# Optimization experiments

Hardware: AMD Instinct MI355X
Metric: run time of the kernel (lower is better)

## Reference

```python
import jax, jax.numpy as jnp
import numpy as np

EXTENT = 1.0  # kernel-point influence radius (init kwarg 'extent')
B, N, M, H, K, F, C = 4, 16384, 16384, 32, 15, 64, 64


def setup_inputs() -> dict:
    key = jax.random.key(0)
    ks = jax.random.split(key, 6)
    points = jax.random.uniform(ks[0], (B, N, 3), dtype=jnp.float32)
    features = jax.random.normal(ks[1], (B, N, F), dtype=jnp.float32)
    output_points = jax.random.uniform(ks[2], (B, M, 3), dtype=jnp.float32)
    neighbor_indices = jax.random.randint(ks[3], (B, M, H), 0, N)
    # kernel point dispositions inside a ball of radius 1.5*extent (load_kernels stand-in)
    k_points = jax.random.uniform(ks[4], (K, 3), minval=-1.0, maxval=1.0, dtype=jnp.float32) * (1.5 * EXTENT) / jnp.sqrt(3.0)
    k_values = jax.random.normal(ks[5], (K, F, C), dtype=jnp.float32) * 0.05
    return {
        'points': points, 'features': features, 'output_points': output_points,
        'k_points': k_points, 'k_values': k_values, 'neighbor_indices': neighbor_indices,
    }


def reference(points, features, output_points, k_points, k_values, neighbor_indices):
    b, m, h = neighbor_indices.shape
    idx = neighbor_indices.reshape(b, m * h, 1)
    # batched gather (tf.gather batch_dims=1)
    neigh_pts = jnp.take_along_axis(points, idx, axis=1).reshape(b, m, h, 3)
    neigh_feat = jnp.take_along_axis(features, idx, axis=1).reshape(b, m, h, -1)
    # relative coords to each output point, then to each kernel point
    rel = neigh_pts - output_points[:, :, None, :]                # [B,M,H,3]
    diff = rel[:, :, :, None, :] - k_points                       # [B,M,H,K,3]
    sq_d = jnp.sum(diff * diff, axis=-1)                          # [B,M,H,K]
    # linear influence
    w = jnp.maximum(1.0 - jnp.sqrt(sq_d) / EXTENT, 0.0)           # [B,M,H,K]
    # weight neighbor features per kernel point, then apply per-kernel linear map, sum over K
    wf = jnp.einsum('bmhk,bmhf->bmkf', w, neigh_feat)             # [B,M,K,F]
    out = jnp.einsum('bmkf,kfc->bmc', wf, k_values)               # [B,M,C]
    return out
```

## Files before the change

### kernel.cpp

```cpp
#include <hip/hip_runtime.h>

#define BATCH 4
#define NPTS 16384
#define MPTS 16384
#define NH 32
#define NK 15
#define NF 64
#define NC 64
#define MT 16

typedef short short8 __attribute__((ext_vector_type(8)));
typedef float floatx4 __attribute__((ext_vector_type(4)));

__device__ __forceinline__ unsigned short f2bf(float x) {
    unsigned int u = __builtin_bit_cast(unsigned int, x);
    u = u + 0x7FFFu + ((u >> 16) & 1u);
    return (unsigned short)(u >> 16);
}

__global__ void feat_cvt_kernel(const float* __restrict__ src, unsigned short* __restrict__ dst) {
    const int gid = blockIdx.x * 256 + threadIdx.x;
    const size_t base = (size_t)gid * 8;
    float4 a = *(const float4*)(src + base);
    float4 b = *(const float4*)(src + base + 4);
    uint4 o;
    o.x = (unsigned)f2bf(a.x) | ((unsigned)f2bf(a.y) << 16);
    o.y = (unsigned)f2bf(a.z) | ((unsigned)f2bf(a.w) << 16);
    o.z = (unsigned)f2bf(b.x) | ((unsigned)f2bf(b.y) << 16);
    o.w = (unsigned)f2bf(b.z) | ((unsigned)f2bf(b.w) << 16);
    *(uint4*)(dst + base) = o;
}

__global__ void vprep_kernel(const float* __restrict__ kv, unsigned short* __restrict__ vp) {
    const int gid = blockIdx.x * 256 + threadIdx.x;
    const int lane = gid & 63;
    const int ct   = (gid >> 6) & 3;
    const int kk   = gid >> 8;
    const int c    = ct * 16 + (lane & 15);
    const int kap0 = kk * 32 + (lane >> 4) * 8;
    unsigned int o[4];
    #pragma unroll
    for (int jj = 0; jj < 4; jj++) {
        unsigned short lo, hi;
        {
            const int kap = kap0 + jj * 2;
            const int f = kap >> 4, k = kap & 15;
            lo = (k < NK) ? f2bf(kv[((size_t)(k * NF + f)) * NC + c]) : (unsigned short)0;
        }
        {
            const int kap = kap0 + jj * 2 + 1;
            const int f = kap >> 4, k = kap & 15;
            hi = (k < NK) ? f2bf(kv[((size_t)(k * NF + f)) * NC + c]) : (unsigned short)0;
        }
        o[jj] = (unsigned)lo | ((unsigned)hi << 16);
    }
    *(uint4*)(vp + (size_t)gid * 8) = make_uint4(o[0], o[1], o[2], o[3]);
}

__global__ __launch_bounds__(256, 3) void kpconv_kernel(
    const float* __restrict__ points,
    const unsigned short* __restrict__ featbf,
    const float* __restrict__ outpts,
    const float* __restrict__ kpts,
    const unsigned short* __restrict__ vp,
    const int*   __restrict__ nbr,
    float* __restrict__ out)
{
    __shared__ unsigned short wf_s[MT * 1032];
    __shared__ unsigned short feat_s[4 * 32 * 36];
    __shared__ unsigned short w_s[4 * 16 * 40];
    __shared__ int   idx_s[MT * 32];
    __shared__ float kp_s[48];

    const int tid   = threadIdx.x;
    const int batch = blockIdx.x >> 10;
    const int m0    = (blockIdx.x & 1023) << 4;

    if (tid < 45) kp_s[tid] = kpts[tid];
    {
        const size_t nb = (size_t)(batch * MPTS + m0) * NH;
        idx_s[tid]       = nbr[nb + tid];
        idx_s[256 + tid] = nbr[nb + 256 + tid];
    }
    __syncthreads();

    const int g    = tid >> 6;
    const int lane = tid & 63;
    const int cl   = lane & 15;
    const int q    = lane >> 4;

    for (int r = 0; r < 4; r++) {
        {
            const int pl = tid >> 6;
            const int h  = tid & 31;
            const int ktop = (tid >> 5) & 1;
            const int p  = r * 4 + pl;
            const int id = idx_s[p * 32 + h];
            const size_t pb = ((size_t)(batch * NPTS) + id) * 3;
            const size_t ob = (size_t)(batch * MPTS + m0 + p) * 3;
            const float rx = points[pb + 0] - outpts[ob + 0];
            const float ry = points[pb + 1] - outpts[ob + 1];
            const float rz = points[pb + 2] - outpts[ob + 2];
            #pragma unroll
            for (int kk2 = 0; kk2 < 8; kk2++) {
                const int k = ktop * 8 + kk2;
                float w = 0.f;
                if (k < NK) {
                    const float dx = rx - kp_s[k * 3 + 0];
                    const float dy = ry - kp_s[k * 3 + 1];
                    const float dz = rz - kp_s[k * 3 + 2];
                    const float d  = sqrtf(dx * dx + dy * dy + dz * dz);
                    w = fmaxf(1.f - d, 0.f);
                }
                w_s[(pl * 16 + k) * 40 + h] = f2bf(w);
            }
        }
        {
            const int rowId = tid >> 1, qh = tid & 1;
            const int pl = rowId >> 5, h = rowId & 31;
            const int id = idx_s[(r * 4 + pl) * 32 + h];
            const unsigned short* src = featbf + ((size_t)(batch * NPTS) + id) * NF;
            unsigned short* dsth = &feat_s[(pl * 32 + h) * 36];
            #pragma unroll
            for (int cch = 0; cch < 2; cch++) {
                const int off = qh * 8 + cch * 16;
                uint4 d = *(const uint4*)(src + off);
                *(uint2*)(dsth + off)     = make_uint2(d.x, d.y);
                *(uint2*)(dsth + off + 4) = make_uint2(d.z, d.w);
            }
        }
        __syncthreads();

        const int p = r * 4 + g;
        const uint4 ua = *(const uint4*)&w_s[(g * 16 + cl) * 40 + q * 8];
        const short8 af = __builtin_bit_cast(short8, ua);

        #pragma unroll
        for (int t = 0; t < 2; t++) {
            const int fl = t * 16 + cl;
            const int fb = (g * 32 + q * 8) * 36 + fl;
            short8 bfv;
            #pragma unroll
            for (int j = 0; j < 8; j++) bfv[j] = (short)feat_s[fb + j * 36];
            floatx4 d = {0.f, 0.f, 0.f, 0.f};
            d = __builtin_amdgcn_mfma_f32_16x16x32_bf16(af, bfv, d, 0, 0, 0);
            const unsigned int lo = (unsigned)f2bf(d[0]) | ((unsigned)f2bf(d[1]) << 16);
            const unsigned int hi = (unsigned)f2bf(d[2]) | ((unsigned)f2bf(d[3]) << 16);
            *(uint2*)&wf_s[p * 1032 + (t * 16 + cl) * 16 + q * 4] = make_uint2(lo, hi);
        }
        __syncthreads();

        {
            const int rowId = tid >> 1, qh = tid & 1;
            const int pl = rowId >> 5, h = rowId & 31;
            const int id = idx_s[(r * 4 + pl) * 32 + h];
            const unsigned short* src = featbf + ((size_t)(batch * NPTS) + id) * NF + 32;
            unsigned short* dsth = &feat_s[(pl * 32 + h) * 36];
            #pragma unroll
            for (int cch = 0; cch < 2; cch++) {
                const int off = qh * 8 + cch * 16;
                uint4 d = *(const uint4*)(src + off);
                *(uint2*)(dsth + off)     = make_uint2(d.x, d.y);
                *(uint2*)(dsth + off + 4) = make_uint2(d.z, d.w);
            }
        }
        __syncthreads();

        #pragma unroll
        for (int t = 0; t < 2; t++) {
            const int fl = t * 16 + cl;
            const int fb = (g * 32 + q * 8) * 36 + fl;
            short8 bfv;
            #pragma unroll
            for (int j = 0; j < 8; j++) bfv[j] = (short)feat_s[fb + j * 36];
            floatx4 d = {0.f, 0.f, 0.f, 0.f};
            d = __builtin_amdgcn_mfma_f32_16x16x32_bf16(af, bfv, d, 0, 0, 0);
            const unsigned int lo = (unsigned)f2bf(d[0]) | ((unsigned)f2bf(d[1]) << 16);
            const unsigned int hi = (unsigned)f2bf(d[2]) | ((unsigned)f2bf(d[3]) << 16);
            *(uint2*)&wf_s[p * 1032 + ((2 + t) * 16 + cl) * 16 + q * 4] = make_uint2(lo, hi);
        }
        __syncthreads();
    }

    floatx4 acc = {0.f, 0.f, 0.f, 0.f};
    #pragma unroll 8
    for (int kk = 0; kk < 32; kk++) {
        const uint4 uA = *(const uint4*)&wf_s[cl * 1032 + kk * 32 + q * 8];
        const uint4 uB = *(const uint4*)(vp + ((size_t)((kk * 4 + g) * 64 + lane)) * 8);
        acc = __builtin_amdgcn_mfma_f32_16x16x32_bf16(
            __builtin_bit_cast(short8, uA), __builtin_bit_cast(short8, uB), acc, 0, 0, 0);
    }

    #pragma unroll
    for (int ri = 0; ri < 4; ri++) {
        out[((size_t)(batch * MPTS + m0 + q * 4 + ri)) * NC + g * 16 + cl] = acc[ri];
    }
}

extern "C" void kernel_launch(void* const* d_in, const int* in_sizes, int n_in,
                              void* d_out, int out_size, void* d_ws, size_t ws_size,
                              hipStream_t stream) {
    const float* points   = (const float*)d_in[0];
    const float* features = (const float*)d_in[1];
    const float* outpts   = (const float*)d_in[2];
    const float* kpts     = (const float*)d_in[3];
    const float* kvals    = (const float*)d_in[4];
    const int*   nbr      = (const int*)d_in[5];
    float* out = (float*)d_out;

    unsigned short* vp     = (unsigned short*)d_ws;
    unsigned short* featbf = (unsigned short*)((char*)d_ws + 131072);

    vprep_kernel<<<32, 256, 0, stream>>>(kvals, vp);
    feat_cvt_kernel<<<2048, 256, 0, stream>>>(features, featbf);

    const int blocks = BATCH * (MPTS / MT);
    kpconv_kernel<<<blocks, 256, 0, stream>>>(points, featbf, outpts, kpts, vp, nbr, out);
}
```

Baseline: 159.9 us.

## Restructure LDS layouts with transposed feature staging, swizzled WF buffer, in-register weights

```diff
diff --git a/kernel.cpp b/kernel.cpp
--- a/kernel.cpp
+++ b/kernel.cpp
@@ -16,6 +16,11 @@
     unsigned int u = __builtin_bit_cast(unsigned int, x);
     u = u + 0x7FFFu + ((u >> 16) & 1u);
     return (unsigned short)(u >> 16);
+}
+
+__device__ __forceinline__ unsigned pack_trunc(float lo, float hi) {
+    return __builtin_amdgcn_perm(__builtin_bit_cast(unsigned, hi),
+                                 __builtin_bit_cast(unsigned, lo), 0x07060302u);
 }
 
 __global__ void feat_cvt_kernel(const float* __restrict__ src, unsigned short* __restrict__ dst) {
@@ -66,17 +71,20 @@
     const int*   __restrict__ nbr,
     float* __restrict__ out)
 {
-    __shared__ unsigned short wf_s[MT * 1032];
-    __shared__ unsigned short feat_s[4 * 32 * 36];
-    __shared__ unsigned short w_s[4 * 16 * 40];
-    __shared__ int   idx_s[MT * 32];
+    __shared__ unsigned short awf[32 * 512];
+    __shared__ unsigned short feat_s[4 * 1288];
+    __shared__ float4 rel_s[4 * 32];
+    __shared__ int   idx_s[512];
+    __shared__ float opt_s[48];
     __shared__ float kp_s[48];
 
     const int tid   = threadIdx.x;
     const int batch = blockIdx.x >> 10;
     const int m0    = (blockIdx.x & 1023) << 4;
 
-    if (tid < 45) kp_s[tid] = kpts[tid];
+    if (tid < 48) kp_s[tid] = (tid < 45) ? kpts[tid] : 1e9f;
+    if (tid >= 64 && tid < 112)
+        opt_s[tid - 64] = outpts[(size_t)(batch * MPTS + m0) * 3 + (tid - 64)];
     {
         const size_t nb = (size_t)(batch * MPTS + m0) * NH;
         idx_s[tid]       = nbr[nb + tid];
@@ -90,106 +98,118 @@
     const int q    = lane >> 4;
 
     for (int r = 0; r < 4; r++) {
-        {
-            const int pl = tid >> 6;
-            const int h  = tid & 31;
-            const int ktop = (tid >> 5) & 1;
-            const int p  = r * 4 + pl;
-            const int id = idx_s[p * 32 + h];
-            const size_t pb = ((size_t)(batch * NPTS) + id) * 3;
-            const size_t ob = (size_t)(batch * MPTS + m0 + p) * 3;
-            const float rx = points[pb + 0] - outpts[ob + 0];
-            const float ry = points[pb + 1] - outpts[ob + 1];
-            const float rz = points[pb + 2] - outpts[ob + 2];
+        const int spl = tid >> 6;
+        const int sa  = tid & 15;
+        const int sfc = (tid >> 4) & 3;
+        const int srow = (r * 4 + spl) * 32 + sa * 2;
+        const int id0 = idx_s[srow], id1 = idx_s[srow + 1];
+        const unsigned short* s0p = featbf + ((size_t)(batch * NPTS) + id0) * NF + sfc * 8;
+        const unsigned short* s1p = featbf + ((size_t)(batch * NPTS) + id1) * NF + sfc * 8;
+        unsigned short* dp = &feat_s[spl * 1288 + (sfc * 8) * 40 + sa * 2];
+
+        {
+            uint4 ra = *(const uint4*)s0p;
+            uint4 rb = *(const uint4*)s1p;
+            *(unsigned*)(dp + 0 * 40) = __builtin_amdgcn_perm(rb.x, ra.x, 0x05040100u);
+            *(unsigned*)(dp + 1 * 40) = __builtin_amdgcn_perm(rb.x, ra.x, 0x07060302u);
+            *(unsigned*)(dp + 2 * 40) = __builtin_amdgcn_perm(rb.y, ra.y, 0x05040100u);
+            *(unsigned*)(dp + 3 * 40) = __builtin_amdgcn_perm(rb.y, ra.y, 0x07060302u);
+            *(unsigned*)(dp + 4 * 40) = __builtin_amdgcn_perm(rb.z, ra.z, 0x05040100u);
+            *(unsigned*)(dp + 5 * 40) = __builtin_amdgcn_perm(rb.z, ra.z, 0x07060302u);
+            *(unsigned*)(dp + 6 * 40) = __builtin_amdgcn_perm(rb.w, ra.w, 0x05040100u);
+            *(unsigned*)(dp + 7 * 40) = __builtin_amdgcn_perm(rb.w, ra.w, 0x07060302u);
+        }
+        if (tid < 128) {
+            const int rpl = tid >> 5, rh = tid & 31;
+            const int rid = idx_s[(r * 4 + rpl) * 32 + rh];
+            const float* pp = points + ((size_t)(batch * NPTS) + rid) * 3;
+            const int p = r * 4 + rpl;
+            rel_s[rpl * 32 + rh] = make_float4(pp[0] - opt_s[p * 3 + 0],
+                                               pp[1] - opt_s[p * 3 + 1],
+                                               pp[2] - opt_s[p * 3 + 2], 0.f);
+        }
+        __syncthreads();
+
+        const int p = r * 4 + g;
+        short8 af;
+        {
+            const float kx = kp_s[cl * 3 + 0];
+            const float ky = kp_s[cl * 3 + 1];
+            const float kz = kp_s[cl * 3 + 2];
+            float wv[8];
             #pragma unroll
-            for (int kk2 = 0; kk2 < 8; kk2++) {
-                const int k = ktop * 8 + kk2;
-                float w = 0.f;
-                if (k < NK) {
-                    const float dx = rx - kp_s[k * 3 + 0];
-                    const float dy = ry - kp_s[k * 3 + 1];
-                    const float dz = rz - kp_s[k * 3 + 2];
-                    const float d  = sqrtf(dx * dx + dy * dy + dz * dz);
-                    w = fmaxf(1.f - d, 0.f);
-                }
-                w_s[(pl * 16 + k) * 40 + h] = f2bf(w);
+            for (int j = 0; j < 8; j++) {
+                const float4 rr = rel_s[g * 32 + q * 8 + j];
+                const float dx = rr.x - kx, dy = rr.y - ky, dz = rr.z - kz;
+                const float d = sqrtf(dx * dx + dy * dy + dz * dz);
+                wv[j] = fmaxf(1.f - d, 0.f);
             }
-        }
-        {
-            const int rowId = tid >> 1, qh = tid & 1;
-            const int pl = rowId >> 5, h = rowId & 31;
-            const int id = idx_s[(r * 4 + pl) * 32 + h];
-            const unsigned short* src = featbf + ((size_t)(batch * NPTS) + id) * NF;
-            unsigned short* dsth = &feat_s[(pl * 32 + h) * 36];
-            #pragma unroll
-            for (int cch = 0; cch < 2; cch++) {
-                const int off = qh * 8 + cch * 16;
-                uint4 d = *(const uint4*)(src + off);
-                *(uint2*)(dsth + off)     = make_uint2(d.x, d.y);
-                *(uint2*)(dsth + off + 4) = make_uint2(d.z, d.w);
-            }
-        }
-        __syncthreads();
-
-        const int p = r * 4 + g;
-        const uint4 ua = *(const uint4*)&w_s[(g * 16 + cl) * 40 + q * 8];
-        const short8 af = __builtin_bit_cast(short8, ua);
-
+            uint4 ua;
+            ua.x = pack_trunc(wv[0], wv[1]);
+            ua.y = pack_trunc(wv[2], wv[3]);
+            ua.z = pack_trunc(wv[4], wv[5]);
+            ua.w = pack_trunc(wv[6], wv[7]);
+            af = __builtin_bit_cast(short8, ua);
+        }
         #pragma unroll
         for (int t = 0; t < 2; t++) {
-            const int fl = t * 16 + cl;
-            const int fb = (g * 32 + q * 8) * 36 + fl;
-            short8 bfv;
-            #pragma unroll
-            for (int j = 0; j < 8; j++) bfv[j] = (short)feat_s[fb + j * 36];
-            floatx4 d = {0.f, 0.f, 0.f, 0.f};
-            d = __builtin_amdgcn_mfma_f32_16x16x32_bf16(af, bfv, d, 0, 0, 0);
-            const unsigned int lo = (unsigned)f2bf(d[0]) | ((unsigned)f2bf(d[1]) << 16);
-            const unsigned int hi = (unsigned)f2bf(d[2]) | ((unsigned)f2bf(d[3]) << 16);
-            *(uint2*)&wf_s[p * 1032 + (t * 16 + cl) * 16 + q * 4] = make_uint2(lo, hi);
-        }
-        __syncthreads();
-
-        {
-            const int rowId = tid >> 1, qh = tid & 1;
-            const int pl = rowId >> 5, h = rowId & 31;
-            const int id = idx_s[(r * 4 + pl) * 32 + h];
-            const unsigned short* src = featbf + ((size_t)(batch * NPTS) + id) * NF + 32;
-            unsigned short* dsth = &feat_s[(pl * 32 + h) * 36];
-            #pragma unroll
-            for (int cch = 0; cch < 2; cch++) {
-                const int off = qh * 8 + cch * 16;
-                uint4 d = *(const uint4*)(src + off);
-                *(uint2*)(dsth + off)     = make_uint2(d.x, d.y);
-                *(uint2*)(dsth + off + 4) = make_uint2(d.z, d.w);
-            }
+            const uint4 ub = *(const uint4*)&feat_s[g * 1288 + (t * 16 + cl) * 40 + q * 8];
+            floatx4 dd = {0.f, 0.f, 0.f, 0.f};
+            dd = __builtin_amdgcn_mfma_f32_16x16x32_bf16(af, __builtin_bit_cast(short8, ub), dd, 0, 0, 0);
+            const int kk    = 8 * t + (cl >> 1);
+            const int q2    = (2 * cl + (q >> 1)) & 3;
+            const int chunk = (p ^ (kk & 15)) | (q2 << 4);
+            unsigned* wp = (unsigned*)awf + kk * 256 + chunk * 4 + (q & 1) * 2;
+            wp[0] = pack_trunc(dd[0], dd[1]);
+            wp[1] = pack_trunc(dd[2], dd[3]);
+        }
+        __syncthreads();
+
+        {
+            uint4 ra = *(const uint4*)(s0p + 32);
+            uint4 rb = *(const uint4*)(s1p + 32);
+            *(unsigned*)(dp + 0 * 40) = __builtin_amdgcn_perm(rb.x, ra.x, 0x05040100u);
+            *(unsigned*)(dp + 1 * 40) = __builtin_amdgcn_perm(rb.x, ra.x, 0x07060302u);
+            *(unsigned*)(dp + 2 * 40) = __builtin_amdgcn_perm(rb.y, ra.y, 0x05040100u);
+            *(unsigned*)(dp + 3 * 40) = __builtin_amdgcn_perm(rb.y, ra.y, 0x07060302u);
+            *(unsigned*)(dp + 4 * 40) = __builtin_amdgcn_perm(rb.z, ra.z, 0x05040100u);
+            *(unsigned*)(dp + 5 * 40) = __builtin_amdgcn_perm(rb.z, ra.z, 0x07060302u);
+            *(unsigned*)(dp + 6 * 40) = __builtin_amdgcn_perm(rb.w, ra.w, 0x05040100u);
+            *(unsigned*)(dp + 7 * 40) = __builtin_amdgcn_perm(rb.w, ra.w, 0x07060302u);
         }
         __syncthreads();
 
         #pragma unroll
-        for (int t = 0; t < 2; t++) {
-            const int fl = t * 16 + cl;
-            const int fb = (g * 32 + q * 8) * 36 + fl;
-            short8 bfv;
-            #pragma unroll
-            for (int j = 0; j < 8; j++) bfv[j] = (short)feat_s[fb + j * 36];
-            floatx4 d = {0.f, 0.f, 0.f, 0.f};
-            d = __builtin_amdgcn_mfma_f32_16x16x32_bf16(af, bfv, d, 0, 0, 0);
-            const unsigned int lo = (unsigned)f2bf(d[0]) | ((unsigned)f2bf(d[1]) << 16);
-            const unsigned int hi = (unsigned)f2bf(d[2]) | ((unsigned)f2bf(d[3]) << 16);
-            *(uint2*)&wf_s[p * 1032 + ((2 + t) * 16 + cl) * 16 + q * 4] = make_uint2(lo, hi);
-        }
-        __syncthreads();
-    }
-
-    floatx4 acc = {0.f, 0.f, 0.f, 0.f};
+        for (int t = 2; t < 4; t++) {
+            const uint4 ub = *(const uint4*)&feat_s[g * 1288 + ((t - 2) * 16 + cl) * 40 + q * 8];
+            floatx4 dd = {0.f, 0.f, 0.f, 0.f};
+            dd = __builtin_amdgcn_mfma_f32_16x16x32_bf16(af, __builtin_bit_cast(short8, ub), dd, 0, 0, 0);
+            const int kk    = 8 * t + (cl >> 1);
+            const int q2    = (2 * cl + (q >> 1)) & 3;
+            const int chunk = (p ^ (kk & 15)) | (q2 << 4);
+            unsigned* wp = (unsigned*)awf + kk * 256 + chunk * 4 + (q & 1) * 2;
+            wp[0] = pack_trunc(dd[0], dd[1]);
+            wp[1] = pack_trunc(dd[2], dd[3]);
+        }
+        __syncthreads();
+    }
+
+    floatx4 acc0 = {0.f, 0.f, 0.f, 0.f};
+    floatx4 acc1 = {0.f, 0.f, 0.f, 0.f};
+    const unsigned short* vpg = vp + g * 512 + lane * 8;
     #pragma unroll 8
     for (int kk = 0; kk < 32; kk++) {
-        const uint4 uA = *(const uint4*)&wf_s[cl * 1032 + kk * 32 + q * 8];
-        const uint4 uB = *(const uint4*)(vp + ((size_t)((kk * 4 + g) * 64 + lane)) * 8);
-        acc = __builtin_amdgcn_mfma_f32_16x16x32_bf16(
-            __builtin_bit_cast(short8, uA), __builtin_bit_cast(short8, uB), acc, 0, 0, 0);
-    }
+        const int chunk = ((lane & 15) ^ (kk & 15)) | (lane & 48);
+        const uint4 uA = *(const uint4*)&awf[kk * 512 + chunk * 8];
+        const uint4 uB = *(const uint4*)(vpg + (size_t)kk * 2048);
+        if (kk & 1)
+            acc1 = __builtin_amdgcn_mfma_f32_16x16x32_bf16(
+                __builtin_bit_cast(short8, uA), __builtin_bit_cast(short8, uB), acc1, 0, 0, 0);
+        else
+            acc0 = __builtin_amdgcn_mfma_f32_16x16x32_bf16(
+                __builtin_bit_cast(short8, uA), __builtin_bit_cast(short8, uB), acc0, 0, 0, 0);
+    }
+    const floatx4 acc = acc0 + acc1;
 
     #pragma unroll
     for (int ri = 0; ri < 4; ri++) {
```

Measured after the change: 163.8 us. 1.02x slower.
